# Performance work log

Measured on AMD Instinct MI355X. Metric: run time of the kernel, lower is better.

Reference implementation:

```python
import jax, jax.numpy as jnp
import numpy as np

N_NODES = 50000
N_EDGES = 800000
H = 64      # node_hidden_size
S = 16      # static_feature_size
EF = 16     # edge_feature_size
ATT_IN = 2 * H + 2 * S + EF   # 176
ATT_W = 2 * H + EF            # 144
UPD_IN = 2 * H                # 128
UPD_W = 2 * H                 # 128


def setup_inputs() -> dict:
    key = jax.random.key(0)
    ks = jax.random.split(key, 12)
    x = jax.random.normal(ks[0], (N_NODES, H), dtype=jnp.float32)
    x_s = jax.random.normal(ks[1], (N_NODES, S), dtype=jnp.float32)
    edge_index = jax.random.randint(ks[2], (2, N_EDGES), 0, N_NODES, dtype=jnp.int32)
    edge_features = jax.random.normal(ks[3], (N_EDGES, EF), dtype=jnp.float32)

    def lin(k, out_dim, in_dim):
        lim = 1.0 / np.sqrt(in_dim)
        kw, kb = jax.random.split(k)
        W = jax.random.uniform(kw, (out_dim, in_dim), minval=-lim, maxval=lim, dtype=jnp.float32)
        b = jax.random.uniform(kb, (out_dim,), minval=-lim, maxval=lim, dtype=jnp.float32)
        return W, b

    att_w1, att_b1 = lin(ks[4], ATT_W, ATT_IN)
    att_w2, att_b2 = lin(ks[5], 1, ATT_W)
    upd_w1, upd_b1 = lin(ks[6], UPD_W, UPD_IN)
    upd_w2, upd_b2 = lin(ks[7], H, UPD_W)

    return {
        "x": x, "x_s": x_s, "edge_index": edge_index, "edge_features": edge_features,
        "att_w1": att_w1, "att_b1": att_b1, "att_w2": att_w2, "att_b2": att_b2,
        "upd_w1": upd_w1, "upd_b1": upd_b1, "upd_w2": upd_w2, "upd_b2": upd_b2,
    }


def segment_softmax(scores, segment_ids, num_segments):
    max_scores = jax.ops.segment_max(scores, segment_ids, num_segments=num_segments)
    exp_scores = jnp.exp(scores - max_scores[segment_ids])
    sum_exp = jax.ops.segment_sum(exp_scores, segment_ids, num_segments=num_segments)
    return exp_scores / (sum_exp[segment_ids] + 1e-9)


def reference(x, x_s, edge_index, edge_features,
              att_w1, att_b1, att_w2, att_b2,
              upd_w1, upd_b1, upd_w2, upd_b2):
    num_nodes = x.shape[0]
    src, dst = edge_index[0], edge_index[1]

    # gather per-edge features: [E, 2H+2S+EF]
    att_in = jnp.concatenate(
        [x[src], x[dst], x_s[src], x_s[dst], edge_features], axis=-1)

    # attention MLP (depth=1, relu hidden), squeeze to [E]
    h = jax.nn.relu(att_in @ att_w1.T + att_b1)
    raw = (h @ att_w2.T + att_b2).squeeze(-1)
    raw = jax.nn.leaky_relu(raw)

    attn = segment_softmax(raw, dst, num_nodes)

    # weighted scatter-sum of source hidden feats -> [N, H]
    aggregated = jax.ops.segment_sum(x[src] * attn[:, None], dst, num_segments=num_nodes)

    upd_in = jnp.concatenate([x, aggregated], axis=-1)
    u = jax.nn.relu(upd_in @ upd_w1.T + upd_b1)
    out = u @ upd_w2.T + upd_b2
    return jax.nn.relu(out)
```

## Files before the change

kernel.cpp:

```cpp
#include <hip/hip_runtime.h>
#include <math.h>

#define N_NODES_C 50000
#define E_C       800000
#define ATT_IN_C  176
#define ATT_HID_C 144
#define SCAN_B    98
#define UPD_TILES 3125
#define SC_BLOCKS 512

typedef __attribute__((ext_vector_type(8))) __bf16 bf16x8;
typedef __attribute__((ext_vector_type(4))) float f32x4;

#define O_RAW   0L
#define O_DEG   3201024L
#define O_OFF   3402752L
#define O_CUR   3603456L
#define O_CSR   3804160L
#define O_EFP   10206208L
#define O_XB    35807232L
#define O_XSB   42208256L
#define O_W1B   43809280L
#define O_UW1B  43860992L
#define O_UW2B  43894784L
#define O_AGGB  43912192L
#define O_PSUM  O_AGGB
#define O_BOFF  (O_AGGB + 512L)

__device__ __forceinline__ bf16x8 bzero8() {
    bf16x8 z;
#pragma unroll
    for (int i = 0; i < 8; ++i) z[i] = (__bf16)0.0f;
    return z;
}

__global__ __launch_bounds__(256) void k_deg(const int* __restrict__ ei, int* __restrict__ deg) {
    int e = blockIdx.x * blockDim.x + threadIdx.x;
    if (e < E_C) atomicAdd(&deg[ei[E_C + e]], 1);
}

__global__ __launch_bounds__(256) void k_scan1(const int* __restrict__ deg,
                                               int* __restrict__ psum) {
    __shared__ int red[256];
    int b = blockIdx.x, t = threadIdx.x;
    int i = b * 512 + t * 2;
    int s = 0;
    if (i < N_NODES_C) s += deg[i];
    if (i + 1 < N_NODES_C) s += deg[i + 1];
    red[t] = s;
    __syncthreads();
#pragma unroll
    for (int off = 128; off > 0; off >>= 1) {
        if (t < off) red[t] += red[t + off];
        __syncthreads();
    }
    if (t == 0) psum[b] = red[0];
}

__global__ __launch_bounds__(128) void k_scan2(const int* __restrict__ psum,
                                               int* __restrict__ boff,
                                               int* __restrict__ offsets) {
    __shared__ int sc[128];
    int t = threadIdx.x;
    int v = (t < SCAN_B) ? psum[t] : 0;
    sc[t] = v;
    __syncthreads();
#pragma unroll
    for (int off = 1; off < 128; off <<= 1) {
        int val = sc[t];
        int add = (t >= off) ? sc[t - off] : 0;
        __syncthreads();
        sc[t] = val + add;
        __syncthreads();
    }
    boff[t] = sc[t] - v;
    if (t == SCAN_B - 1) offsets[N_NODES_C] = sc[t];
}

__global__ __launch_bounds__(256) void k_scan3(const int* __restrict__ deg,
                                               const int* __restrict__ boff,
                                               int* __restrict__ offsets,
                                               int* __restrict__ cursor) {
    __shared__ int sc[256];
    int b = blockIdx.x, t = threadIdx.x;
    int i = b * 512 + t * 2;
    int d0 = (i < N_NODES_C) ? deg[i] : 0;
    int d1 = (i + 1 < N_NODES_C) ? deg[i + 1] : 0;
    int s = d0 + d1;
    sc[t] = s;
    __syncthreads();
#pragma unroll
    for (int off = 1; off < 256; off <<= 1) {
        int val = sc[t];
        int add = (t >= off) ? sc[t - off] : 0;
        __syncthreads();
        sc[t] = val + add;
        __syncthreads();
    }
    int excl = boff[b] + sc[t] - s;
    if (i < N_NODES_C)     { offsets[i]     = excl;      cursor[i]     = excl; }
    if (i + 1 < N_NODES_C) { offsets[i + 1] = excl + d0; cursor[i + 1] = excl + d0; }
}

__global__ __launch_bounds__(256) void k_fill(const int* __restrict__ ei,
                                              const float* __restrict__ ef,
                                              int* __restrict__ cursor,
                                              int2* __restrict__ csr,
                                              __bf16* __restrict__ efp) {
    int e = blockIdx.x * blockDim.x + threadIdx.x;
    if (e < E_C) {
        int src  = ei[e];
        int dst  = ei[E_C + e];
        int slot = atomicAdd(&cursor[dst], 1);
        csr[slot] = make_int2(src, dst);
        const float4* pe = (const float4*)(ef + (long)e * 16);
        float4 f0 = pe[0], f1 = pe[1], f2 = pe[2], f3 = pe[3];
        bf16x8 o0, o1;
        o0[0] = (__bf16)f0.x; o0[1] = (__bf16)f0.y; o0[2] = (__bf16)f0.z; o0[3] = (__bf16)f0.w;
        o0[4] = (__bf16)f1.x; o0[5] = (__bf16)f1.y; o0[6] = (__bf16)f1.z; o0[7] = (__bf16)f1.w;
        o1[0] = (__bf16)f2.x; o1[1] = (__bf16)f2.y; o1[2] = (__bf16)f2.z; o1[3] = (__bf16)f2.w;
        o1[4] = (__bf16)f3.x; o1[5] = (__bf16)f3.y; o1[6] = (__bf16)f3.z; o1[7] = (__bf16)f3.w;
        *(bf16x8*)(efp + (long)slot * 16)     = o0;
        *(bf16x8*)(efp + (long)slot * 16 + 8) = o1;
    }
}

__global__ __launch_bounds__(256) void k_cvt(
    const float* __restrict__ x, const float* __restrict__ xs,
    const float* __restrict__ w1, const float* __restrict__ uw1,
    const float* __restrict__ uw2,
    __bf16* __restrict__ xb, __bf16* __restrict__ xsb,
    __bf16* __restrict__ w1b, __bf16* __restrict__ uw1b,
    __bf16* __restrict__ uw2b)
{
    long g = (long)blockIdx.x * 256 + threadIdx.x;
    const long G_X = 400000, G_XS = 500000, G_W1 = 503168, G_UW1 = 505216, G_UW2 = 506240;
    if (g >= G_UW2) return;
    const float* src; __bf16* dst; long off;
    if (g < G_X)        { src = x;   dst = xb;   off = g * 8; }
    else if (g < G_XS)  { src = xs;  dst = xsb;  off = (g - G_X) * 8; }
    else if (g < G_W1)  { src = w1;  dst = w1b;  off = (g - G_XS) * 8; }
    else if (g < G_UW1) { src = uw1; dst = uw1b; off = (g - G_W1) * 8; }
    else                { src = uw2; dst = uw2b; off = (g - G_UW1) * 8; }
    float4 a = *(const float4*)(src + off);
    float4 b = *(const float4*)(src + off + 4);
    bf16x8 o;
    o[0] = (__bf16)a.x; o[1] = (__bf16)a.y; o[2] = (__bf16)a.z; o[3] = (__bf16)a.w;
    o[4] = (__bf16)b.x; o[5] = (__bf16)b.y; o[6] = (__bf16)b.z; o[7] = (__bf16)b.w;
    *(bf16x8*)(dst + off) = o;
}

__device__ __forceinline__ void load_afrags(
    int src, int dst, long t, int mrow, int quad,
    const __bf16* __restrict__ xb, const __bf16* __restrict__ xsb,
    const __bf16* __restrict__ efp,
    bf16x8 a[6])
{
    long p = t * 16 + mrow;
    const __bf16* px = xb + (long)src * 64 + quad * 8;
    const __bf16* pd = xb + (long)dst * 64 + quad * 8;
    a[0] = *(const bf16x8*)(px);
    a[1] = *(const bf16x8*)(px + 32);
    a[2] = *(const bf16x8*)(pd);
    a[3] = *(const bf16x8*)(pd + 32);
    if (quad < 2) {
        a[4] = *(const bf16x8*)(xsb + (long)src * 16 + quad * 8);
        a[5] = *(const bf16x8*)(efp + p * 16 + quad * 8);
    } else {
        a[4] = *(const bf16x8*)(xsb + (long)dst * 16 + (quad - 2) * 8);
        a[5] = bzero8();
    }
}

__global__ __launch_bounds__(256) void k_scores_mfma(
    const __bf16* __restrict__ xb, const __bf16* __restrict__ xsb,
    const __bf16* __restrict__ efp, const __bf16* __restrict__ w1b,
    const int2* __restrict__ csr,
    const float* __restrict__ b1, const float* __restrict__ w2,
    const float* __restrict__ b2, float* __restrict__ raw)
{
    int tid  = threadIdx.x;
    int lane = tid & 63;
    int w    = blockIdx.x * 4 + (tid >> 6);
    const int NT = E_C / 16;
    const int TOT_W = SC_BLOCKS * 4;
    int per = (NT + TOT_W - 1) / TOT_W;
    long t0 = (long)w * per;
    long t1 = t0 + per; if (t1 > NT) t1 = NT;
    if (t0 >= t1) return;

    int mrow = lane & 15;
    int quad = lane >> 4;

    bf16x8 bfr[6][9];
#pragma unroll
    for (int ks = 0; ks < 6; ++ks) {
        int k0 = ks * 32 + quad * 8;
#pragma unroll
        for (int nt = 0; nt < 9; ++nt) {
            int n = nt * 16 + mrow;
            if (k0 + 8 <= ATT_IN_C)
                bfr[ks][nt] = *(const bf16x8*)(w1b + (long)n * ATT_IN_C + k0);
            else
                bfr[ks][nt] = bzero8();
        }
    }

    float b1v[9], w2v[9];
#pragma unroll
    for (int nt = 0; nt < 9; ++nt) {
        int n = nt * 16 + mrow;
        b1v[nt] = b1[n];
        w2v[nt] = w2[n];
    }
    float b2v = b2[0];

    bf16x8 acur[6], anext[6];
    int ns = 0, nd = 0;
    {
        int2 c0 = csr[t0 * 16 + mrow];
        load_afrags(c0.x, c0.y, t0, mrow, quad, xb, xsb, efp, acur);
        if (t0 + 1 < t1) {
            int2 c1 = csr[(t0 + 1) * 16 + mrow];
            load_afrags(c1.x, c1.y, t0 + 1, mrow, quad, xb, xsb, efp, anext);
        }
    }

    for (long t = t0; t < t1; ++t) {
        if (t + 2 < t1) {
            int2 c2 = csr[(t + 2) * 16 + mrow];
            ns = c2.x;
            nd = c2.y;
        }

        f32x4 acc[9];
#pragma unroll
        for (int nt = 0; nt < 9; ++nt) acc[nt] = (f32x4){0.f, 0.f, 0.f, 0.f};

#pragma unroll
        for (int ks = 0; ks < 6; ++ks) {
#pragma unroll
            for (int nt = 0; nt < 9; ++nt) {
                acc[nt] = __builtin_amdgcn_mfma_f32_16x16x32_bf16(
                    acur[ks], bfr[ks][nt], acc[nt], 0, 0, 0);
            }
        }

        float p0 = 0.f, p1 = 0.f, p2 = 0.f, p3 = 0.f;
#pragma unroll
        for (int nt = 0; nt < 9; ++nt) {
            p0 += w2v[nt] * fmaxf(acc[nt][0] + b1v[nt], 0.f);
            p1 += w2v[nt] * fmaxf(acc[nt][1] + b1v[nt], 0.f);
            p2 += w2v[nt] * fmaxf(acc[nt][2] + b1v[nt], 0.f);
            p3 += w2v[nt] * fmaxf(acc[nt][3] + b1v[nt], 0.f);
        }
#pragma unroll
        for (int off = 1; off < 16; off <<= 1) {
            p0 += __shfl_xor(p0, off, 64);
            p1 += __shfl_xor(p1, off, 64);
            p2 += __shfl_xor(p2, off, 64);
            p3 += __shfl_xor(p3, off, 64);
        }
        if (mrow < 4) {
            float v = (mrow == 0) ? p0 : (mrow == 1) ? p1 : (mrow == 2) ? p2 : p3;
            v += b2v;
            v = (v >= 0.f) ? v : 0.01f * v;
            raw[t * 16 + quad * 4 + mrow] = v;
        }

#pragma unroll
        for (int i = 0; i < 6; ++i) acur[i] = anext[i];
        if (t + 2 < t1)
            load_afrags(ns, nd, t + 2, mrow, quad, xb, xsb, efp, anext);
    }
}

__global__ __launch_bounds__(256) void k_agg(
    const __bf16* __restrict__ xb, const int* __restrict__ offsets,
    const int2* __restrict__ csr,
    const float* __restrict__ raw, __bf16* __restrict__ aggb)
{
    int tid = threadIdx.x;
    int wave = tid >> 6, lane = tid & 63;
    int v = blockIdx.x * 4 + wave;
    if (v >= N_NODES_C) return;
    int s0 = offsets[v], s1 = offsets[v + 1];

    float m = -INFINITY;
    for (int p = s0 + lane; p < s1; p += 64) m = fmaxf(m, raw[p]);
#pragma unroll
    for (int off = 32; off > 0; off >>= 1) m = fmaxf(m, __shfl_xor(m, off, 64));

    float acc = 0.f, sum = 0.f;
    for (int p = s0; p < s1; ++p) {
        int src = csr[p].x;
        float w = expf(raw[p] - m);
        sum += w;
        acc += w * (float)xb[(long)src * 64 + lane];
    }
    aggb[(long)v * 64 + lane] = (__bf16)(acc / (sum + 1e-9f));
}

__global__ __launch_bounds__(256) void k_upd_mfma(
    const __bf16* __restrict__ xb, const __bf16* __restrict__ aggb,
    const __bf16* __restrict__ w1b, const float* __restrict__ b1,
    const __bf16* __restrict__ w2b, const float* __restrict__ b2,
    float* __restrict__ out)
{
    __shared__ __bf16 ubuf[4][16 * 136];
    int tid = threadIdx.x, wid = tid >> 6, lane = tid & 63;
    int tile = blockIdx.x * 4 + wid;
    if (tile >= UPD_TILES) return;
    int mrow = lane & 15, quad = lane >> 4;

    long node = (long)tile * 16 + mrow;
    bf16x8 a1[4];
    a1[0] = *(const bf16x8*)(xb + node * 64 + quad * 8);
    a1[1] = *(const bf16x8*)(xb + node * 64 + 32 + quad * 8);
    a1[2] = *(const bf16x8*)(aggb + node * 64 + quad * 8);
    a1[3] = *(const bf16x8*)(aggb + node * 64 + 32 + quad * 8);

    bf16x8 b1f[4][8];
#pragma unroll
    for (int ks = 0; ks < 4; ++ks)
#pragma unroll
        for (int nt = 0; nt < 8; ++nt)
            b1f[ks][nt] = *(const bf16x8*)(w1b + (long)(nt * 16 + mrow) * 128 + ks * 32 + quad * 8);

    f32x4 acc1[8];
#pragma unroll
    for (int nt = 0; nt < 8; ++nt) acc1[nt] = (f32x4){0.f, 0.f, 0.f, 0.f};
#pragma unroll
    for (int ks = 0; ks < 4; ++ks)
#pragma unroll
        for (int nt = 0; nt < 8; ++nt)
            acc1[nt] = __builtin_amdgcn_mfma_f32_16x16x32_bf16(a1[ks], b1f[ks][nt], acc1[nt], 0, 0, 0);

    __bf16* ub = ubuf[wid];
#pragma unroll
    for (int nt = 0; nt < 8; ++nt) {
        float bb = b1[nt * 16 + mrow];
#pragma unroll
        for (int r = 0; r < 4; ++r) {
            float h = fmaxf(acc1[nt][r] + bb, 0.f);
            ub[(quad * 4 + r) * 136 + nt * 16 + mrow] = (__bf16)h;
        }
    }

    bf16x8 a2[4];
#pragma unroll
    for (int ks = 0; ks < 4; ++ks)
        a2[ks] = *(bf16x8*)&ub[mrow * 136 + ks * 32 + quad * 8];

    bf16x8 b2f[4][4];
#pragma unroll
    for (int ks = 0; ks < 4; ++ks)
#pragma unroll
        for (int nt = 0; nt < 4; ++nt)
            b2f[ks][nt] = *(const bf16x8*)(w2b + (long)(nt * 16 + mrow) * 128 + ks * 32 + quad * 8);

    f32x4 acc2[4];
#pragma unroll
    for (int nt = 0; nt < 4; ++nt) acc2[nt] = (f32x4){0.f, 0.f, 0.f, 0.f};
#pragma unroll
    for (int ks = 0; ks < 4; ++ks)
#pragma unroll
        for (int nt = 0; nt < 4; ++nt)
            acc2[nt] = __builtin_amdgcn_mfma_f32_16x16x32_bf16(a2[ks], b2f[ks][nt], acc2[nt], 0, 0, 0);

#pragma unroll
    for (int nt = 0; nt < 4; ++nt) {
        float bb = b2[nt * 16 + mrow];
#pragma unroll
        for (int r = 0; r < 4; ++r) {
            long nodeo = (long)tile * 16 + quad * 4 + r;
            out[nodeo * 64 + nt * 16 + mrow] = fmaxf(acc2[nt][r] + bb, 0.f);
        }
    }
}

extern "C" void kernel_launch(void* const* d_in, const int* in_sizes, int n_in,
                              void* d_out, int out_size, void* d_ws, size_t ws_size,
                              hipStream_t stream) {
    const float* x    = (const float*)d_in[0];
    const float* xs   = (const float*)d_in[1];
    const int*   ei   = (const int*)d_in[2];
    const float* ef   = (const float*)d_in[3];
    const float* aw1  = (const float*)d_in[4];
    const float* ab1  = (const float*)d_in[5];
    const float* aw2  = (const float*)d_in[6];
    const float* ab2  = (const float*)d_in[7];
    const float* uw1  = (const float*)d_in[8];
    const float* ub1  = (const float*)d_in[9];
    const float* uw2  = (const float*)d_in[10];
    const float* ub2  = (const float*)d_in[11];
    float* out = (float*)d_out;

    char* ws = (char*)d_ws;
    float*  raw     = (float*)(ws + O_RAW);
    int*    deg     = (int*)(ws + O_DEG);
    int*    offsets = (int*)(ws + O_OFF);
    int*    cursor  = (int*)(ws + O_CUR);
    int2*   csr     = (int2*)(ws + O_CSR);
    __bf16* efp     = (__bf16*)(ws + O_EFP);
    __bf16* xb      = (__bf16*)(ws + O_XB);
    __bf16* xsb     = (__bf16*)(ws + O_XSB);
    __bf16* w1b     = (__bf16*)(ws + O_W1B);
    __bf16* uw1b    = (__bf16*)(ws + O_UW1B);
    __bf16* uw2b    = (__bf16*)(ws + O_UW2B);
    __bf16* aggb    = (__bf16*)(ws + O_AGGB);
    int*    psum    = (int*)(ws + O_PSUM);
    int*    boff    = (int*)(ws + O_BOFF);

    hipMemsetAsync(deg, 0, N_NODES_C * sizeof(int), stream);
    hipLaunchKernelGGL(k_deg,      dim3((E_C + 255) / 256),       dim3(256), 0, stream, ei, deg);
    hipLaunchKernelGGL(k_scan1,    dim3(SCAN_B),                  dim3(256), 0, stream, deg, psum);
    hipLaunchKernelGGL(k_scan2,    dim3(1),                       dim3(128), 0, stream, psum, boff, offsets);
    hipLaunchKernelGGL(k_scan3,    dim3(SCAN_B),                  dim3(256), 0, stream, deg, boff, offsets, cursor);
    hipLaunchKernelGGL(k_fill,     dim3((E_C + 255) / 256),       dim3(256), 0, stream,
                       ei, ef, cursor, csr, efp);
    hipLaunchKernelGGL(k_cvt,      dim3(1978),                    dim3(256), 0, stream,
                       x, xs, aw1, uw1, uw2, xb, xsb, w1b, uw1b, uw2b);
    hipLaunchKernelGGL(k_scores_mfma, dim3(SC_BLOCKS),            dim3(256), 0, stream,
                       xb, xsb, efp, w1b, csr, ab1, aw2, ab2, raw);
    hipLaunchKernelGGL(k_agg,      dim3((N_NODES_C + 3) / 4),     dim3(256), 0, stream,
                       xb, offsets, csr, raw, aggb);
    hipLaunchKernelGGL(k_upd_mfma, dim3((UPD_TILES + 3) / 4),     dim3(256), 0, stream,
                       xb, aggb, uw1b, ub1, uw2b, ub2, out);
}
```

Before: 415.0 us.

## Index edge features by original edge id and double tiles per scores wave

The fill kernel now writes only an int4 CSR entry (src, dst, edge id) and no longer scatters permuted bf16 edge features. The edge-feature conversion moves into the coalesced k_cvt pass, and the scores kernel gathers edge features by original edge id. The scores kernel also processes two 16-edge tiles per iteration with half as many blocks, giving more independent MFMA chains per wave. The trade-offs are a larger CSR record read by the aggregation kernel, random edge-feature gathers, and higher register pressure from the doubled fragments and accumulators.

```diff
diff --git a/kernel.cpp b/kernel.cpp
--- a/kernel.cpp
+++ b/kernel.cpp
@@ -7,7 +7,6 @@
 #define ATT_HID_C 144
 #define SCAN_B    98
 #define UPD_TILES 3125
-#define SC_BLOCKS 512
 
 typedef __attribute__((ext_vector_type(8))) __bf16 bf16x8;
 typedef __attribute__((ext_vector_type(4))) float f32x4;
@@ -17,13 +16,13 @@
 #define O_OFF   3402752L
 #define O_CUR   3603456L
 #define O_CSR   3804160L
-#define O_EFP   10206208L
-#define O_XB    35807232L
-#define O_XSB   42208256L
-#define O_W1B   43809280L
-#define O_UW1B  43860992L
-#define O_UW2B  43894784L
-#define O_AGGB  43912192L
+#define O_EFB   16605184L
+#define O_XB    42206208L
+#define O_XSB   48607232L
+#define O_W1B   50208256L
+#define O_UW1B  50259968L
+#define O_UW2B  50293760L
+#define O_AGGB  50311168L
 #define O_PSUM  O_AGGB
 #define O_BOFF  (O_AGGB + 512L)
 
@@ -103,43 +102,34 @@
 }
 
 __global__ __launch_bounds__(256) void k_fill(const int* __restrict__ ei,
-                                              const float* __restrict__ ef,
                                               int* __restrict__ cursor,
-                                              int2* __restrict__ csr,
-                                              __bf16* __restrict__ efp) {
+                                              int4* __restrict__ csr) {
     int e = blockIdx.x * blockDim.x + threadIdx.x;
     if (e < E_C) {
         int src  = ei[e];
         int dst  = ei[E_C + e];
         int slot = atomicAdd(&cursor[dst], 1);
-        csr[slot] = make_int2(src, dst);
-        const float4* pe = (const float4*)(ef + (long)e * 16);
-        float4 f0 = pe[0], f1 = pe[1], f2 = pe[2], f3 = pe[3];
-        bf16x8 o0, o1;
-        o0[0] = (__bf16)f0.x; o0[1] = (__bf16)f0.y; o0[2] = (__bf16)f0.z; o0[3] = (__bf16)f0.w;
-        o0[4] = (__bf16)f1.x; o0[5] = (__bf16)f1.y; o0[6] = (__bf16)f1.z; o0[7] = (__bf16)f1.w;
-        o1[0] = (__bf16)f2.x; o1[1] = (__bf16)f2.y; o1[2] = (__bf16)f2.z; o1[3] = (__bf16)f2.w;
-        o1[4] = (__bf16)f3.x; o1[5] = (__bf16)f3.y; o1[6] = (__bf16)f3.z; o1[7] = (__bf16)f3.w;
-        *(bf16x8*)(efp + (long)slot * 16)     = o0;
-        *(bf16x8*)(efp + (long)slot * 16 + 8) = o1;
+        csr[slot] = make_int4(src, dst, e, 0);
     }
 }
 
 __global__ __launch_bounds__(256) void k_cvt(
     const float* __restrict__ x, const float* __restrict__ xs,
-    const float* __restrict__ w1, const float* __restrict__ uw1,
-    const float* __restrict__ uw2,
+    const float* __restrict__ ef, const float* __restrict__ w1,
+    const float* __restrict__ uw1, const float* __restrict__ uw2,
     __bf16* __restrict__ xb, __bf16* __restrict__ xsb,
-    __bf16* __restrict__ w1b, __bf16* __restrict__ uw1b,
-    __bf16* __restrict__ uw2b)
+    __bf16* __restrict__ efb, __bf16* __restrict__ w1b,
+    __bf16* __restrict__ uw1b, __bf16* __restrict__ uw2b)
 {
     long g = (long)blockIdx.x * 256 + threadIdx.x;
-    const long G_X = 400000, G_XS = 500000, G_W1 = 503168, G_UW1 = 505216, G_UW2 = 506240;
+    const long G_X = 400000, G_XS = 500000, G_EF = 2100000,
+               G_W1 = 2103168, G_UW1 = 2105216, G_UW2 = 2106240;
     if (g >= G_UW2) return;
     const float* src; __bf16* dst; long off;
     if (g < G_X)        { src = x;   dst = xb;   off = g * 8; }
     else if (g < G_XS)  { src = xs;  dst = xsb;  off = (g - G_X) * 8; }
-    else if (g < G_W1)  { src = w1;  dst = w1b;  off = (g - G_XS) * 8; }
+    else if (g < G_EF)  { src = ef;  dst = efb;  off = (g - G_XS) * 8; }
+    else if (g < G_W1)  { src = w1;  dst = w1b;  off = (g - G_EF) * 8; }
     else if (g < G_UW1) { src = uw1; dst = uw1b; off = (g - G_W1) * 8; }
     else                { src = uw2; dst = uw2b; off = (g - G_UW1) * 8; }
     float4 a = *(const float4*)(src + off);
@@ -151,12 +141,11 @@
 }
 
 __device__ __forceinline__ void load_afrags(
-    int src, int dst, long t, int mrow, int quad,
+    int src, int dst, int e, int quad,
     const __bf16* __restrict__ xb, const __bf16* __restrict__ xsb,
-    const __bf16* __restrict__ efp,
+    const __bf16* __restrict__ efb,
     bf16x8 a[6])
 {
-    long p = t * 16 + mrow;
     const __bf16* px = xb + (long)src * 64 + quad * 8;
     const __bf16* pd = xb + (long)dst * 64 + quad * 8;
     a[0] = *(const bf16x8*)(px);
@@ -165,7 +154,7 @@
     a[3] = *(const bf16x8*)(pd + 32);
     if (quad < 2) {
         a[4] = *(const bf16x8*)(xsb + (long)src * 16 + quad * 8);
-        a[5] = *(const bf16x8*)(efp + p * 16 + quad * 8);
+        a[5] = *(const bf16x8*)(efb + (long)e * 16 + quad * 8);
     } else {
         a[4] = *(const bf16x8*)(xsb + (long)dst * 16 + (quad - 2) * 8);
         a[5] = bzero8();
@@ -174,20 +163,19 @@
 
 __global__ __launch_bounds__(256) void k_scores_mfma(
     const __bf16* __restrict__ xb, const __bf16* __restrict__ xsb,
-    const __bf16* __restrict__ efp, const __bf16* __restrict__ w1b,
-    const int2* __restrict__ csr,
+    const __bf16* __restrict__ efb, const __bf16* __restrict__ w1b,
+    const int4* __restrict__ csr,
     const float* __restrict__ b1, const float* __restrict__ w2,
     const float* __restrict__ b2, float* __restrict__ raw)
 {
     int tid  = threadIdx.x;
     int lane = tid & 63;
     int w    = blockIdx.x * 4 + (tid >> 6);
-    const int NT = E_C / 16;
-    const int TOT_W = SC_BLOCKS * 4;
-    int per = (NT + TOT_W - 1) / TOT_W;
-    long t0 = (long)w * per;
-    long t1 = t0 + per; if (t1 > NT) t1 = NT;
-    if (t0 >= t1) return;
+    const int NP = E_C / 32;
+    int per = (NP + 1023) / 1024;
+    long j0 = (long)w * per;
+    long j1 = j0 + per; if (j1 > NP) j1 = NP;
+    if (j0 >= j1) return;
 
     int mrow = lane & 15;
     int quad = lane >> 4;
@@ -215,69 +203,91 @@
     }
     float b2v = b2[0];
 
-    bf16x8 acur[6], anext[6];
-    int ns = 0, nd = 0;
+    bf16x8 curA[6], curB[6], nxtA[6], nxtB[6];
+    int4 cA = make_int4(0, 0, 0, 0), cB = cA;
     {
-        int2 c0 = csr[t0 * 16 + mrow];
-        load_afrags(c0.x, c0.y, t0, mrow, quad, xb, xsb, efp, acur);
-        if (t0 + 1 < t1) {
-            int2 c1 = csr[(t0 + 1) * 16 + mrow];
-            load_afrags(c1.x, c1.y, t0 + 1, mrow, quad, xb, xsb, efp, anext);
-        }
-    }
-
-    for (long t = t0; t < t1; ++t) {
-        if (t + 2 < t1) {
-            int2 c2 = csr[(t + 2) * 16 + mrow];
-            ns = c2.x;
-            nd = c2.y;
-        }
-
-        f32x4 acc[9];
-#pragma unroll
-        for (int nt = 0; nt < 9; ++nt) acc[nt] = (f32x4){0.f, 0.f, 0.f, 0.f};
+        int4 e0 = csr[j0 * 32 + mrow];
+        int4 e1 = csr[j0 * 32 + 16 + mrow];
+        load_afrags(e0.x, e0.y, e0.z, quad, xb, xsb, efb, curA);
+        load_afrags(e1.x, e1.y, e1.z, quad, xb, xsb, efb, curB);
+        if (j0 + 1 < j1) {
+            int4 f0 = csr[(j0 + 1) * 32 + mrow];
+            int4 f1 = csr[(j0 + 1) * 32 + 16 + mrow];
+            load_afrags(f0.x, f0.y, f0.z, quad, xb, xsb, efb, nxtA);
+            load_afrags(f1.x, f1.y, f1.z, quad, xb, xsb, efb, nxtB);
+        }
+    }
+
+    for (long j = j0; j < j1; ++j) {
+        if (j + 2 < j1) {
+            cA = csr[(j + 2) * 32 + mrow];
+            cB = csr[(j + 2) * 32 + 16 + mrow];
+        }
+
+        f32x4 accA[9], accB[9];
+#pragma unroll
+        for (int nt = 0; nt < 9; ++nt) {
+            accA[nt] = (f32x4){0.f, 0.f, 0.f, 0.f};
+            accB[nt] = (f32x4){0.f, 0.f, 0.f, 0.f};
+        }
 
 #pragma unroll
         for (int ks = 0; ks < 6; ++ks) {
 #pragma unroll
             for (int nt = 0; nt < 9; ++nt) {
-                acc[nt] = __builtin_amdgcn_mfma_f32_16x16x32_bf16(
-                    acur[ks], bfr[ks][nt], acc[nt], 0, 0, 0);
+                accA[nt] = __builtin_amdgcn_mfma_f32_16x16x32_bf16(
+                    curA[ks], bfr[ks][nt], accA[nt], 0, 0, 0);
+                accB[nt] = __builtin_amdgcn_mfma_f32_16x16x32_bf16(
+                    curB[ks], bfr[ks][nt], accB[nt], 0, 0, 0);
             }
         }
 
-        float p0 = 0.f, p1 = 0.f, p2 = 0.f, p3 = 0.f;
+        float pA0 = 0.f, pA1 = 0.f, pA2 = 0.f, pA3 = 0.f;
+        float pB0 = 0.f, pB1 = 0.f, pB2 = 0.f, pB3 = 0.f;
 #pragma unroll
         for (int nt = 0; nt < 9; ++nt) {
-            p0 += w2v[nt] * fmaxf(acc[nt][0] + b1v[nt], 0.f);
-            p1 += w2v[nt] * fmaxf(acc[nt][1] + b1v[nt], 0.f);
-            p2 += w2v[nt] * fmaxf(acc[nt][2] + b1v[nt], 0.f);
-            p3 += w2v[nt] * fmaxf(acc[nt][3] + b1v[nt], 0.f);
+            pA0 += w2v[nt] * fmaxf(accA[nt][0] + b1v[nt], 0.f);
+            pA1 += w2v[nt] * fmaxf(accA[nt][1] + b1v[nt], 0.f);
+            pA2 += w2v[nt] * fmaxf(accA[nt][2] + b1v[nt], 0.f);
+            pA3 += w2v[nt] * fmaxf(accA[nt][3] + b1v[nt], 0.f);
+            pB0 += w2v[nt] * fmaxf(accB[nt][0] + b1v[nt], 0.f);
+            pB1 += w2v[nt] * fmaxf(accB[nt][1] + b1v[nt], 0.f);
+            pB2 += w2v[nt] * fmaxf(accB[nt][2] + b1v[nt], 0.f);
+            pB3 += w2v[nt] * fmaxf(accB[nt][3] + b1v[nt], 0.f);
         }
 #pragma unroll
         for (int off = 1; off < 16; off <<= 1) {
-            p0 += __shfl_xor(p0, off, 64);
-            p1 += __shfl_xor(p1, off, 64);
-            p2 += __shfl_xor(p2, off, 64);
-            p3 += __shfl_xor(p3, off, 64);
+            pA0 += __shfl_xor(pA0, off, 64);
+            pA1 += __shfl_xor(pA1, off, 64);
+            pA2 += __shfl_xor(pA2, off, 64);
+            pA3 += __shfl_xor(pA3, off, 64);
+            pB0 += __shfl_xor(pB0, off, 64);
+            pB1 += __shfl_xor(pB1, off, 64);
+            pB2 += __shfl_xor(pB2, off, 64);
+            pB3 += __shfl_xor(pB3, off, 64);
         }
         if (mrow < 4) {
-            float v = (mrow == 0) ? p0 : (mrow == 1) ? p1 : (mrow == 2) ? p2 : p3;
-            v += b2v;
-            v = (v >= 0.f) ? v : 0.01f * v;
-            raw[t * 16 + quad * 4 + mrow] = v;
-        }
-
-#pragma unroll
-        for (int i = 0; i < 6; ++i) acur[i] = anext[i];
-        if (t + 2 < t1)
-            load_afrags(ns, nd, t + 2, mrow, quad, xb, xsb, efp, anext);
+            float vA = (mrow == 0) ? pA0 : (mrow == 1) ? pA1 : (mrow == 2) ? pA2 : pA3;
+            float vB = (mrow == 0) ? pB0 : (mrow == 1) ? pB1 : (mrow == 2) ? pB2 : pB3;
+            vA += b2v; vB += b2v;
+            vA = (vA >= 0.f) ? vA : 0.01f * vA;
+            vB = (vB >= 0.f) ? vB : 0.01f * vB;
+            raw[(j * 2) * 16 + quad * 4 + mrow]     = vA;
+            raw[(j * 2 + 1) * 16 + quad * 4 + mrow] = vB;
+        }
+
+#pragma unroll
+        for (int i = 0; i < 6; ++i) { curA[i] = nxtA[i]; curB[i] = nxtB[i]; }
+        if (j + 2 < j1) {
+            load_afrags(cA.x, cA.y, cA.z, quad, xb, xsb, efb, nxtA);
+            load_afrags(cB.x, cB.y, cB.z, quad, xb, xsb, efb, nxtB);
+        }
     }
 }
 
 __global__ __launch_bounds__(256) void k_agg(
     const __bf16* __restrict__ xb, const int* __restrict__ offsets,
-    const int2* __restrict__ csr,
+    const int4* __restrict__ csr,
     const float* __restrict__ raw, __bf16* __restrict__ aggb)
 {
     int tid = threadIdx.x;
@@ -401,8 +411,8 @@
     int*    deg     = (int*)(ws + O_DEG);
     int*    offsets = (int*)(ws + O_OFF);
     int*    cursor  = (int*)(ws + O_CUR);
-    int2*   csr     = (int2*)(ws + O_CSR);
-    __bf16* efp     = (__bf16*)(ws + O_EFP);
+    int4*   csr     = (int4*)(ws + O_CSR);
+    __bf16* efb     = (__bf16*)(ws + O_EFB);
     __bf16* xb      = (__bf16*)(ws + O_XB);
     __bf16* xsb     = (__bf16*)(ws + O_XSB);
     __bf16* w1b     = (__bf16*)(ws + O_W1B);
@@ -418,11 +428,11 @@
     hipLaunchKernelGGL(k_scan2,    dim3(1),                       dim3(128), 0, stream, psum, boff, offsets);
     hipLaunchKernelGGL(k_scan3,    dim3(SCAN_B),                  dim3(256), 0, stream, deg, boff, offsets, cursor);
     hipLaunchKernelGGL(k_fill,     dim3((E_C + 255) / 256),       dim3(256), 0, stream,
-                       ei, ef, cursor, csr, efp);
-    hipLaunchKernelGGL(k_cvt,      dim3(1978),                    dim3(256), 0, stream,
-                       x, xs, aw1, uw1, uw2, xb, xsb, w1b, uw1b, uw2b);
-    hipLaunchKernelGGL(k_scores_mfma, dim3(SC_BLOCKS),            dim3(256), 0, stream,
-                       xb, xsb, efp, w1b, csr, ab1, aw2, ab2, raw);
+                       ei, cursor, csr);
+    hipLaunchKernelGGL(k_cvt,      dim3(8228),                    dim3(256), 0, stream,
+                       x, xs, ef, aw1, uw1, uw2, xb, xsb, efb, w1b, uw1b, uw2b);
+    hipLaunchKernelGGL(k_scores_mfma, dim3(256),                  dim3(256), 0, stream,
+                       xb, xsb, efb, w1b, csr, ab1, aw2, ab2, raw);
     hipLaunchKernelGGL(k_agg,      dim3((N_NODES_C + 3) / 4),     dim3(256), 0, stream,
                        xb, offsets, csr, raw, aggb);
     hipLaunchKernelGGL(k_upd_mfma, dim3((UPD_TILES + 3) / 4),     dim3(256), 0, stream,
```

Measured after the change: 400.9 us. -3.4%, faster.
